# Kernel tuning notes

Hardware: AMD Instinct MI355X
Metric: run time of the kernel (lower is better)

## Reference

```python
import jax, jax.numpy as jnp
import numpy as np

N_NODES = 100000
N_EDGES = 1250000
IN_CH = 64
HID = 64
HID2 = 32
N_CLS = 2


def _lin_init(key, fan_in, fan_out):
    return jax.random.normal(key, (fan_in, fan_out), dtype=jnp.float32) / np.sqrt(fan_in)


def setup_inputs() -> dict:
    key = jax.random.key(0)
    ks = jax.random.split(key, 12)
    x = jax.random.normal(ks[0], (N_NODES, IN_CH), dtype=jnp.float32)
    edge_index = jax.random.randint(ks[1], (2, N_EDGES), 0, N_NODES, dtype=jnp.int64 if jax.config.jax_enable_x64 else jnp.int32)
    return {
        "x": x,
        "edge_index": edge_index,
        # SAGEConv1: lin_l (applied to neighbor mean, with bias), lin_r (root, no bias)
        "w1_l": _lin_init(ks[2], IN_CH, HID),
        "b1": jnp.zeros((HID,), jnp.float32),
        "w1_r": _lin_init(ks[3], IN_CH, HID),
        # SAGEConv2
        "w2_l": _lin_init(ks[4], HID, HID2),
        "b2": jnp.zeros((HID2,), jnp.float32),
        "w2_r": _lin_init(ks[5], HID, HID2),
        # proj Linear(32, 32)
        "wp": _lin_init(ks[6], HID2, HID2),
        "bp": jnp.zeros((HID2,), jnp.float32),
        # clf Linear(32, 2)
        "wc": _lin_init(ks[7], HID2, N_CLS),
        "bc": jnp.zeros((N_CLS,), jnp.float32),
    }


def _sage_conv(h, src, dst, w_l, b_l, w_r):
    # PyG SAGEConv (mean aggr): out = lin_l(mean_{j in N(i)} x_j) + lin_r(x_i)
    msg = h[src]  # [E, d] gather of source-node features
    agg = jax.ops.segment_sum(msg, dst, num_segments=N_NODES)  # [N, d]
    cnt = jax.ops.segment_sum(jnp.ones((src.shape[0],), h.dtype), dst, num_segments=N_NODES)
    mean = agg / jnp.maximum(cnt, 1.0)[:, None]
    return mean @ w_l + b_l + h @ w_r


def reference(x, edge_index, w1_l, b1, w1_r, w2_l, b2, w2_r, wp, bp, wc, bc):
    src, dst = edge_index[0], edge_index[1]
    h = jax.nn.relu(_sage_conv(x, src, dst, w1_l, b1, w1_r))   # [N, 64]
    h = jax.nn.relu(_sage_conv(h, src, dst, w2_l, b2, w2_r))   # [N, 32]
    z = h @ wp + bp                                            # [N, 32]
    logits = z @ wc + bc                                       # [N, 2]
    return (logits, z)
```

## Files before the change

kernel.cpp:

```cpp
#include <hip/hip_runtime.h>

#define NN 100000
#define NE 1250000
#define NE4 (NE / 4)
#define CAP 40
#define PART 12500

#define GEG 128
#define GXG 196
#define GTG (GEG + GXG)

typedef unsigned short u16;
typedef unsigned char u8;
typedef unsigned int u32;

__device__ inline float b2f(u16 h) { return __uint_as_float(((u32)h) << 16); }
__device__ inline u16 f2b(float f) {
    u32 u = __float_as_uint(f);
    u = (u + 0x7FFFu + ((u >> 16) & 1u)) >> 16;
    return (u16)u;
}

__device__ inline u8 f2e4(float f) {
    u32 s = (__float_as_uint(f) >> 24) & 0x80u;
    float a = fminf(fabsf(f), 448.0f);
    u32 ua = __float_as_uint(a);
    ua += 0x7FFFFu + ((ua >> 20) & 1u);
    int em = (int)(ua >> 20) - (120 << 3);
    em = (em < 8) ? 0 : em;
    return (u8)(s | (u32)em);
}

__device__ inline void dec4acc(uchar4 vc, float ms,
                               float& a0, float& a1, float& a2, float& a3) {
    u32 raw;
    __builtin_memcpy(&raw, &vc, 4);
    u32 p01 = __builtin_amdgcn_perm(0u, raw, 0x010c000cu) & 0xff00ff00u;
    u32 p23 = __builtin_amdgcn_perm(0u, raw, 0x030c020cu) & 0xff00ff00u;
    u32 u01 = (p01 & 0x80008000u) | ((p01 & 0x7f007f00u) >> 4);
    u32 u23 = (p23 & 0x80008000u) | ((p23 & 0x7f007f00u) >> 4);
    a0 = fmaf(__uint_as_float(u01 << 16),        ms, a0);
    a1 = fmaf(__uint_as_float(u01 & 0xffff0000u), ms, a1);
    a2 = fmaf(__uint_as_float(u23 << 16),        ms, a2);
    a3 = fmaf(__uint_as_float(u23 & 0xffff0000u), ms, a3);
}

#define MS_SCALE 0x1p120f

__global__ void __launch_bounds__(512) k1_fused(
        const int* __restrict__ src, const int* __restrict__ dst,
        int* __restrict__ cnt, int* __restrict__ ell,
        const float* __restrict__ x,
        const float* __restrict__ w1l, const float* __restrict__ b1,
        const float* __restrict__ w1r,
        u8* __restrict__ y1f8, u16* __restrict__ s1h) {
    __shared__ float sx[8][8][64];

    int g = blockIdx.x >> 3;
    int p = blockIdx.x & 7;
    int e_lo = (g * GEG) / GTG;
    int e_hi = ((g + 1) * GEG) / GTG;

    if (e_hi > e_lo) {
        int eb = (int)(((long)e_lo * NE4) / GEG);
        int ee = (int)(((long)(e_lo + 1) * NE4) / GEG);
        int lo = p * PART, hi = lo + PART;
        const int4* s4p = (const int4*)src;
        const int4* d4p = (const int4*)dst;
        for (int i = eb + threadIdx.x; i < ee; i += 512) {
            int4 d4 = d4p[i];
            int4 s4 = s4p[i];
            if (d4.x >= lo && d4.x < hi) {
                int t = atomicAdd(&cnt[d4.x], 1);
                if (t < CAP) ell[(size_t)d4.x * CAP + t] = s4.x;
            }
            if (d4.y >= lo && d4.y < hi) {
                int t = atomicAdd(&cnt[d4.y], 1);
                if (t < CAP) ell[(size_t)d4.y * CAP + t] = s4.y;
            }
            if (d4.z >= lo && d4.z < hi) {
                int t = atomicAdd(&cnt[d4.z], 1);
                if (t < CAP) ell[(size_t)d4.z * CAP + t] = s4.z;
            }
            if (d4.w >= lo && d4.w < hi) {
                int t = atomicAdd(&cnt[d4.w], 1);
                if (t < CAP) ell[(size_t)d4.w * CAP + t] = s4.w;
            }
        }
        return;
    }

    int blk  = (g - e_lo) * 8 + p;
    int w    = threadIdx.x >> 6;
    int lane = threadIdx.x & 63;
    int n0   = (blk * 8 + w) * 8;
    if (n0 >= NN) return;

#pragma unroll
    for (int r = 0; r < 8; ++r) sx[w][r][lane] = x[(size_t)(n0 + r) * 64 + lane];
    __builtin_amdgcn_wave_barrier();

    float accy[8], accs[8];
    float bias = b1[lane];
#pragma unroll
    for (int r = 0; r < 8; ++r) { accy[r] = 0.0f; accs[r] = bias; }

#pragma unroll
    for (int k4 = 0; k4 < 16; ++k4) {
        int k = k4 * 4;
        float wl0 = w1l[(k + 0) * 64 + lane], wr0 = w1r[(k + 0) * 64 + lane];
        float wl1 = w1l[(k + 1) * 64 + lane], wr1 = w1r[(k + 1) * 64 + lane];
        float wl2 = w1l[(k + 2) * 64 + lane], wr2 = w1r[(k + 2) * 64 + lane];
        float wl3 = w1l[(k + 3) * 64 + lane], wr3 = w1r[(k + 3) * 64 + lane];
#pragma unroll
        for (int r = 0; r < 8; ++r) {
            float4 xv = *(const float4*)&sx[w][r][k];
            accy[r] = fmaf(xv.x, wl0, accy[r]); accs[r] = fmaf(xv.x, wr0, accs[r]);
            accy[r] = fmaf(xv.y, wl1, accy[r]); accs[r] = fmaf(xv.y, wr1, accs[r]);
            accy[r] = fmaf(xv.z, wl2, accy[r]); accs[r] = fmaf(xv.z, wr2, accs[r]);
            accy[r] = fmaf(xv.w, wl3, accy[r]); accs[r] = fmaf(xv.w, wr3, accs[r]);
        }
    }

#pragma unroll
    for (int r = 0; r < 8; ++r) {
        y1f8[(size_t)(n0 + r) * 64 + lane] = f2e4(accy[r]);
        s1h[(size_t)(n0 + r) * 64 + lane]  = f2b(accs[r]);
    }
}

__global__ void __launch_bounds__(512) k2_gather1_xform2(
        const u8* __restrict__ y1f8, u16* s1h, u16* __restrict__ y2p,
        const int* __restrict__ cnt, const int* __restrict__ ell,
        const float* __restrict__ w2l, const float* __restrict__ b2v,
        const float* __restrict__ w2r) {
    __shared__ float lwt[2 * 32 * 68];
    __shared__ float lb2[32];
    __shared__ float sh[8][64];

    for (int i = threadIdx.x; i < 2 * 2048; i += 512) {
        int sel = i >> 11;
        int rem = i & 2047;
        int k   = rem >> 5;
        int col = rem & 31;
        float v = sel ? w2r[rem] : w2l[rem];
        lwt[sel * 2176 + col * 68 + k] = v;
    }
    if (threadIdx.x < 32) lb2[threadIdx.x] = b2v[threadIdx.x];
    __syncthreads();

    int w    = threadIdx.x >> 6;
    int lane = threadIdx.x & 63;
    int node = blockIdx.x * 8 + w;
    int grp = lane >> 4, fl = lane & 15;

    int raw = (lane < CAP) ? ell[(size_t)node * CAP + lane] : 0;
    int dg  = cnt[node];
    ushort4 sv = ((const ushort4*)(s1h + (size_t)node * 64))[fl];

    int dgc = dg < CAP ? dg : CAP;
    int ids = (lane < dgc) ? raw : node;

    int j0 = grp, j1 = 4+grp, j2 = 8+grp, j3 = 12+grp, j4 = 16+grp, j5 = 20+grp;
    int i0 = __shfl(ids, j0), i1 = __shfl(ids, j1), i2 = __shfl(ids, j2);
    int i3 = __shfl(ids, j3), i4 = __shfl(ids, j4), i5 = __shfl(ids, j5);
    uchar4 v0 = ((const uchar4*)(y1f8 + (size_t)i0 * 64))[fl];
    uchar4 v1 = ((const uchar4*)(y1f8 + (size_t)i1 * 64))[fl];
    uchar4 v2 = ((const uchar4*)(y1f8 + (size_t)i2 * 64))[fl];
    uchar4 v3 = ((const uchar4*)(y1f8 + (size_t)i3 * 64))[fl];
    uchar4 v4 = ((const uchar4*)(y1f8 + (size_t)i4 * 64))[fl];
    uchar4 v5 = ((const uchar4*)(y1f8 + (size_t)i5 * 64))[fl];

    float ms0 = (j0 < dgc) ? MS_SCALE : 0.0f;
    float ms1 = (j1 < dgc) ? MS_SCALE : 0.0f;
    float ms2 = (j2 < dgc) ? MS_SCALE : 0.0f;
    float ms3 = (j3 < dgc) ? MS_SCALE : 0.0f;
    float ms4 = (j4 < dgc) ? MS_SCALE : 0.0f;
    float ms5 = (j5 < dgc) ? MS_SCALE : 0.0f;

    float a0 = 0.f, a1 = 0.f, a2 = 0.f, a3 = 0.f;
    dec4acc(v0, ms0, a0, a1, a2, a3);
    dec4acc(v1, ms1, a0, a1, a2, a3);
    dec4acc(v2, ms2, a0, a1, a2, a3);
    dec4acc(v3, ms3, a0, a1, a2, a3);
    dec4acc(v4, ms4, a0, a1, a2, a3);
    dec4acc(v5, ms5, a0, a1, a2, a3);

    for (int j = 24; j < dgc; j += 4) {
        int jj = j + grp;
        int s0 = __shfl(ids, jj);
        float m = (jj < dgc) ? MS_SCALE : 0.0f;
        uchar4 u = ((const uchar4*)(y1f8 + (size_t)s0 * 64))[fl];
        dec4acc(u, m, a0, a1, a2, a3);
    }

    a0 += __shfl_xor(a0, 16); a1 += __shfl_xor(a1, 16);
    a2 += __shfl_xor(a2, 16); a3 += __shfl_xor(a3, 16);
    a0 += __shfl_xor(a0, 32); a1 += __shfl_xor(a1, 32);
    a2 += __shfl_xor(a2, 32); a3 += __shfl_xor(a3, 32);

    float inv = 1.0f / (float)(dg > 1 ? dg : 1);
    float h0 = fmaxf(a0 * inv + b2f(sv.x), 0.0f);
    float h1 = fmaxf(a1 * inv + b2f(sv.y), 0.0f);
    float h2 = fmaxf(a2 * inv + b2f(sv.z), 0.0f);
    float h3 = fmaxf(a3 * inv + b2f(sv.w), 0.0f);

    if (lane < 16) *(float4*)&sh[w][fl * 4] = make_float4(h0, h1, h2, h3);
    __builtin_amdgcn_wave_barrier();

    int col = lane & 31;
    int sel = lane >> 5;
    const float* WT = &lwt[sel * 2176 + col * 68];
    float acc = sel ? lb2[col] : 0.0f;
#pragma unroll
    for (int k4 = 0; k4 < 16; ++k4) {
        float4 wv = *(const float4*)(WT + k4 * 4);
        float4 hv = *(const float4*)&sh[w][k4 * 4];
        acc = fmaf(hv.x, wv.x, acc);
        acc = fmaf(hv.y, wv.y, acc);
        acc = fmaf(hv.z, wv.z, acc);
        acc = fmaf(hv.w, wv.w, acc);
    }
    u16 r = f2b(acc);
    if (sel == 0) y2p[(size_t)node * 32 + col] = r;
    else          s1h[(size_t)node * 64 + 32 + col] = r;
}

__global__ void __launch_bounds__(512) k3_gather2(
        const u16* __restrict__ y2p, const u16* __restrict__ s1h,
        const int* __restrict__ cnt, const int* __restrict__ ell,
        const float* __restrict__ wp, const float* __restrict__ bp,
        const float* __restrict__ wc, const float* __restrict__ bc,
        float* __restrict__ logits, float* __restrict__ zout) {
    __shared__ float lwpT[32 * 36];
    __shared__ float sh2[8][32];

    for (int i = threadIdx.x; i < 1024; i += 512) {
        int k = i >> 5, col = i & 31;
        lwpT[col * 36 + k] = wp[i];
    }
    __syncthreads();

    int w    = threadIdx.x >> 6;
    int lane = threadIdx.x & 63;
    int node = blockIdx.x * 8 + w;
    int grp = lane >> 3, fl = lane & 7;
    int col = lane & 31;

    int raw = (lane < CAP) ? ell[(size_t)node * CAP + lane] : 0;
    int dg  = cnt[node];
    float s2f = b2f(s1h[(size_t)node * 64 + 32 + col]);

    int dgc = dg < CAP ? dg : CAP;
    int ids = (lane < dgc) ? raw : node;

    int j0 = grp, j1 = 8 + grp, j2 = 16 + grp, j3 = 24 + grp;
    int i0 = __shfl(ids, j0), i1 = __shfl(ids, j1);
    int i2 = __shfl(ids, j2), i3 = __shfl(ids, j3);
    ushort4 v0 = ((const ushort4*)(y2p + (size_t)i0 * 32))[fl];
    ushort4 v1 = ((const ushort4*)(y2p + (size_t)i1 * 32))[fl];
    ushort4 v2 = {0,0,0,0}, v3 = {0,0,0,0};
    if (dgc > 16) v2 = ((const ushort4*)(y2p + (size_t)i2 * 32))[fl];
    if (dgc > 24) v3 = ((const ushort4*)(y2p + (size_t)i3 * 32))[fl];

    float m0 = (j0 < dgc) ? 1.0f : 0.0f;
    float m1 = (j1 < dgc) ? 1.0f : 0.0f;
    float m2 = (j2 < dgc) ? 1.0f : 0.0f;
    float m3 = (j3 < dgc) ? 1.0f : 0.0f;
    float a0 = m0*b2f(v0.x) + m1*b2f(v1.x) + m2*b2f(v2.x) + m3*b2f(v3.x);
    float a1 = m0*b2f(v0.y) + m1*b2f(v1.y) + m2*b2f(v2.y) + m3*b2f(v3.y);
    float a2 = m0*b2f(v0.z) + m1*b2f(v1.z) + m2*b2f(v2.z) + m3*b2f(v3.z);
    float a3 = m0*b2f(v0.w) + m1*b2f(v1.w) + m2*b2f(v2.w) + m3*b2f(v3.w);

    for (int j = 32; j < dgc; j += 8) {
        int jj = j + grp;
        int s0 = __shfl(ids, jj);
        float m = (jj < dgc) ? 1.0f : 0.0f;
        ushort4 u = ((const ushort4*)(y2p + (size_t)s0 * 32))[fl];
        a0 += m * b2f(u.x); a1 += m * b2f(u.y);
        a2 += m * b2f(u.z); a3 += m * b2f(u.w);
    }

    a0 += __shfl_xor(a0, 8);  a1 += __shfl_xor(a1, 8);
    a2 += __shfl_xor(a2, 8);  a3 += __shfl_xor(a3, 8);
    a0 += __shfl_xor(a0, 16); a1 += __shfl_xor(a1, 16);
    a2 += __shfl_xor(a2, 16); a3 += __shfl_xor(a3, 16);
    a0 += __shfl_xor(a0, 32); a1 += __shfl_xor(a1, 32);
    a2 += __shfl_xor(a2, 32); a3 += __shfl_xor(a3, 32);

    float inv = 1.0f / (float)(dg > 1 ? dg : 1);

    int fsrc = col >> 2;
    float q0 = __shfl(a0, fsrc), q1 = __shfl(a1, fsrc);
    float q2 = __shfl(a2, fsrc), q3 = __shfl(a3, fsrc);
    int e = col & 3;
    float meanv = (e == 0 ? q0 : e == 1 ? q1 : e == 2 ? q2 : q3) * inv;

    float h2 = fmaxf(meanv + s2f, 0.0f);
    if (lane < 32) sh2[w][col] = h2;
    __builtin_amdgcn_wave_barrier();

    float z = bp[col];
#pragma unroll
    for (int k4 = 0; k4 < 8; ++k4) {
        float4 wv = *(const float4*)&lwpT[col * 36 + k4 * 4];
        float4 hv = *(const float4*)&sh2[w][k4 * 4];
        z = fmaf(hv.x, wv.x, z);
        z = fmaf(hv.y, wv.y, z);
        z = fmaf(hv.z, wv.z, z);
        z = fmaf(hv.w, wv.w, z);
    }
    if (lane < 32) zout[(size_t)node * 32 + lane] = z;

    float p0 = (lane < 32) ? z * wc[col * 2 + 0] : 0.0f;
    float p1 = (lane < 32) ? z * wc[col * 2 + 1] : 0.0f;
#pragma unroll
    for (int d = 1; d < 64; d <<= 1) {
        p0 += __shfl_xor(p0, d);
        p1 += __shfl_xor(p1, d);
    }
    if (lane == 0) {
        logits[(size_t)node * 2 + 0] = p0 + bc[0];
        logits[(size_t)node * 2 + 1] = p1 + bc[1];
    }
}

extern "C" void kernel_launch(void* const* d_in, const int* in_sizes, int n_in,
                              void* d_out, int out_size, void* d_ws, size_t ws_size,
                              hipStream_t stream) {
    const float* x    = (const float*)d_in[0];
    const int*   ei   = (const int*)d_in[1];
    const float* w1l  = (const float*)d_in[2];
    const float* b1   = (const float*)d_in[3];
    const float* w1r  = (const float*)d_in[4];
    const float* w2l  = (const float*)d_in[5];
    const float* b2   = (const float*)d_in[6];
    const float* w2r  = (const float*)d_in[7];
    const float* wp   = (const float*)d_in[8];
    const float* bp   = (const float*)d_in[9];
    const float* wc   = (const float*)d_in[10];
    const float* bc   = (const float*)d_in[11];

    const int* src = ei;
    const int* dst = ei + NE;

    char* base = (char*)d_ws;
    int* cnt  = (int*)base;
    int* ell  = (int*)(base + 400000);
    u8*  y1f8 = (u8*)(base + 16400000);
    u16* s1h  = (u16*)(base + 22800000);
    u16* y2p  = (u16*)(base + 35600000);

    float* out_logits = (float*)d_out;
    float* out_z      = (float*)d_out + (size_t)NN * 2;

    hipMemsetAsync(cnt, 0, (size_t)NN * sizeof(int), stream);

    k1_fused<<<GTG * 8, 512, 0, stream>>>(src, dst, cnt, ell,
                                          x, w1l, b1, w1r, y1f8, s1h);

    k2_gather1_xform2<<<NN / 8, 512, 0, stream>>>(y1f8, s1h, y2p, cnt, ell,
                                                  w2l, b2, w2r);

    k3_gather2<<<NN / 8, 512, 0, stream>>>(y2p, s1h, cnt, ell, wp, bp, wc, bc,
                                           out_logits, out_z);
}
```

Measured before the change: 187.7 us.

## Split fused edge-fill/xform kernel into separate kernels with nontemporal edge loads

Splits the combined kernel, which interleaved ELL-fill blocks and layer-1 transform blocks, into two kernels that run one after the other: a dense transform kernel and an edge-bucketing fill kernel. The fill kernel reads src/dst with nontemporal loads so the streamed edge list does not pollute the cache. This gives up the overlap between atomic-heavy fill work and compute-heavy transform work in exchange for simpler, uniform kernels, and adds one extra launch.

```diff
diff --git a/kernel.cpp b/kernel.cpp
--- a/kernel.cpp
+++ b/kernel.cpp
@@ -5,14 +5,12 @@
 #define NE4 (NE / 4)
 #define CAP 40
 #define PART 12500
-
-#define GEG 128
-#define GXG 196
-#define GTG (GEG + GXG)
+#define NCHUNK 128
 
 typedef unsigned short u16;
 typedef unsigned char u8;
 typedef unsigned int u32;
+typedef int iv4 __attribute__((ext_vector_type(4)));
 
 __device__ inline float b2f(u16 h) { return __uint_as_float(((u32)h) << 16); }
 __device__ inline u16 f2b(float f) {
@@ -47,53 +45,16 @@
 
 #define MS_SCALE 0x1p120f
 
-__global__ void __launch_bounds__(512) k1_fused(
-        const int* __restrict__ src, const int* __restrict__ dst,
-        int* __restrict__ cnt, int* __restrict__ ell,
+__global__ void __launch_bounds__(512) kx_xform1(
         const float* __restrict__ x,
         const float* __restrict__ w1l, const float* __restrict__ b1,
         const float* __restrict__ w1r,
         u8* __restrict__ y1f8, u16* __restrict__ s1h) {
     __shared__ float sx[8][8][64];
 
-    int g = blockIdx.x >> 3;
-    int p = blockIdx.x & 7;
-    int e_lo = (g * GEG) / GTG;
-    int e_hi = ((g + 1) * GEG) / GTG;
-
-    if (e_hi > e_lo) {
-        int eb = (int)(((long)e_lo * NE4) / GEG);
-        int ee = (int)(((long)(e_lo + 1) * NE4) / GEG);
-        int lo = p * PART, hi = lo + PART;
-        const int4* s4p = (const int4*)src;
-        const int4* d4p = (const int4*)dst;
-        for (int i = eb + threadIdx.x; i < ee; i += 512) {
-            int4 d4 = d4p[i];
-            int4 s4 = s4p[i];
-            if (d4.x >= lo && d4.x < hi) {
-                int t = atomicAdd(&cnt[d4.x], 1);
-                if (t < CAP) ell[(size_t)d4.x * CAP + t] = s4.x;
-            }
-            if (d4.y >= lo && d4.y < hi) {
-                int t = atomicAdd(&cnt[d4.y], 1);
-                if (t < CAP) ell[(size_t)d4.y * CAP + t] = s4.y;
-            }
-            if (d4.z >= lo && d4.z < hi) {
-                int t = atomicAdd(&cnt[d4.z], 1);
-                if (t < CAP) ell[(size_t)d4.z * CAP + t] = s4.z;
-            }
-            if (d4.w >= lo && d4.w < hi) {
-                int t = atomicAdd(&cnt[d4.w], 1);
-                if (t < CAP) ell[(size_t)d4.w * CAP + t] = s4.w;
-            }
-        }
-        return;
-    }
-
-    int blk  = (g - e_lo) * 8 + p;
     int w    = threadIdx.x >> 6;
     int lane = threadIdx.x & 63;
-    int n0   = (blk * 8 + w) * 8;
+    int n0   = ((int)blockIdx.x * 8 + w) * 8;
     if (n0 >= NN) return;
 
 #pragma unroll
@@ -126,6 +87,38 @@
     for (int r = 0; r < 8; ++r) {
         y1f8[(size_t)(n0 + r) * 64 + lane] = f2e4(accy[r]);
         s1h[(size_t)(n0 + r) * 64 + lane]  = f2b(accs[r]);
+    }
+}
+
+__global__ void __launch_bounds__(512) kf_fill(
+        const int* __restrict__ src, const int* __restrict__ dst,
+        int* __restrict__ cnt, int* __restrict__ ell) {
+    int p = blockIdx.x & 7;
+    int c = blockIdx.x >> 3;
+    int lo = p * PART, hi = lo + PART;
+    int cb = (int)(((long)c * NE4) / NCHUNK);
+    int ce = (int)(((long)(c + 1) * NE4) / NCHUNK);
+    const iv4* s4p = (const iv4*)src;
+    const iv4* d4p = (const iv4*)dst;
+    for (int i = cb + (int)threadIdx.x; i < ce; i += 512) {
+        iv4 d4 = __builtin_nontemporal_load(&d4p[i]);
+        iv4 s4 = __builtin_nontemporal_load(&s4p[i]);
+        if (d4.x >= lo && d4.x < hi) {
+            int t = atomicAdd(&cnt[d4.x], 1);
+            if (t < CAP) ell[(size_t)d4.x * CAP + t] = s4.x;
+        }
+        if (d4.y >= lo && d4.y < hi) {
+            int t = atomicAdd(&cnt[d4.y], 1);
+            if (t < CAP) ell[(size_t)d4.y * CAP + t] = s4.y;
+        }
+        if (d4.z >= lo && d4.z < hi) {
+            int t = atomicAdd(&cnt[d4.z], 1);
+            if (t < CAP) ell[(size_t)d4.z * CAP + t] = s4.z;
+        }
+        if (d4.w >= lo && d4.w < hi) {
+            int t = atomicAdd(&cnt[d4.w], 1);
+            if (t < CAP) ell[(size_t)d4.w * CAP + t] = s4.w;
+        }
     }
 }
 
@@ -356,8 +349,9 @@
 
     hipMemsetAsync(cnt, 0, (size_t)NN * sizeof(int), stream);
 
-    k1_fused<<<GTG * 8, 512, 0, stream>>>(src, dst, cnt, ell,
-                                          x, w1l, b1, w1r, y1f8, s1h);
+    kx_xform1<<<(NN + 63) / 64, 512, 0, stream>>>(x, w1l, b1, w1r, y1f8, s1h);
+
+    kf_fill<<<8 * NCHUNK, 512, 0, stream>>>(src, dst, cnt, ell);
 
     k2_gather1_xform2<<<NN / 8, 512, 0, stream>>>(y1f8, s1h, y2p, cnt, ell,
                                                   w2l, b2, w2r);
```

Result: slower. 207.8 us (+10.7%).
